# Kernel tuning notes

Hardware: AMD Instinct MI355X
Metric: run time of the kernel (lower is better)

Reference implementation:

```python
import jax, jax.numpy as jnp
import numpy as np

D = 128  # inputs / head dim

def setup_inputs() -> dict:
    key = jax.random.key(0)
    ks = jax.random.split(key, 7)
    B, S = 4, 4096
    s = 1.0 / np.sqrt(D)
    return {
        "x": jax.random.normal(ks[0], (B, S, D), dtype=jnp.float32),
        "Wq": jax.random.normal(ks[1], (D, D), dtype=jnp.float32) * s,
        "bq": jax.random.normal(ks[2], (D,), dtype=jnp.float32) * s,
        "Wk": jax.random.normal(ks[3], (D, D), dtype=jnp.float32) * s,
        "bk": jax.random.normal(ks[4], (D,), dtype=jnp.float32) * s,
        "Wv": jax.random.normal(ks[5], (D, D), dtype=jnp.float32) * s,
        "bv": jax.random.normal(ks[6], (D,), dtype=jnp.float32) * s,
    }

def reference(x, Wq, bq, Wk, bk, Wv, bv):
    B, S, d = x.shape
    # nn.Linear: y = x @ W^T + b
    q = jnp.einsum('bsd,ed->bse', x, Wq) + bq
    k = jnp.einsum('bsd,ed->bse', x, Wk) + bk
    v = jnp.einsum('bsd,ed->bse', x, Wv) + bv
    scores = jnp.einsum('bse,bte->bst', q, k) / jnp.sqrt(jnp.asarray(d, x.dtype))
    attn = jax.nn.softmax(scores, axis=-1)
    out = jnp.einsum('bst,bte->bse', attn, v)
    return out.reshape(B, S * d)
```

## Files before the change

### kernel.cpp

```cpp
#include <hip/hip_runtime.h>
#include <hip/hip_bf16.h>

typedef __bf16 bf16x8 __attribute__((ext_vector_type(8)));
typedef __bf16 bf16x4 __attribute__((ext_vector_type(4)));
typedef float  f32x4  __attribute__((ext_vector_type(4)));
typedef float  f32x16 __attribute__((ext_vector_type(16)));
typedef _Float16 f16x4 __attribute__((ext_vector_type(4)));

#define NB 4
#define SEQ 4096
#define DIM 128

static __device__ __forceinline__ unsigned int bf16bits(__bf16 h) {
    return (unsigned int)__builtin_bit_cast(unsigned short, h);
}

#define GLOAD_LDS16(g, s) __builtin_amdgcn_global_load_lds(                    \
    (const __attribute__((address_space(1))) void*)(g),                        \
    (__attribute__((address_space(3))) void*)(s), 16, 0, 0)

__global__ __launch_bounds__(256) void wconv(
    const float* __restrict__ Wq, const float* __restrict__ Wk,
    const float* __restrict__ Wv,
    __bf16* __restrict__ Wh, __bf16* __restrict__ Wl)
{
    int idx = blockIdx.x * 256 + threadIdx.x;
    int which = idx >> 12;
    int off = (idx & 4095) * 4;
    const float* W = which == 0 ? Wq : (which == 1 ? Wk : Wv);
    float4 v = *(const float4*)(W + off);
    bf16x4 h, lo;
    h[0] = (__bf16)v.x; h[1] = (__bf16)v.y; h[2] = (__bf16)v.z; h[3] = (__bf16)v.w;
    lo[0] = (__bf16)(v.x - (float)h[0]);
    lo[1] = (__bf16)(v.y - (float)h[1]);
    lo[2] = (__bf16)(v.z - (float)h[2]);
    lo[3] = (__bf16)(v.w - (float)h[3]);
    *(bf16x4*)(Wh + which * 16384 + off) = h;
    *(bf16x4*)(Wl + which * 16384 + off) = lo;
}

union QkvSh {
    float  xs[64][132];
    __bf16 vbuf[64][200];
};

__global__ __launch_bounds__(256) void qkv_proj3(
    const float* __restrict__ x,
    const __bf16* __restrict__ Whg, const __bf16* __restrict__ Wlg,
    const float* __restrict__ bq, const float* __restrict__ bk,
    const float* __restrict__ bv,
    __bf16* __restrict__ Q, __bf16* __restrict__ K, __bf16* __restrict__ Vt)
{
    __shared__ QkvSh sh;
    const int t  = threadIdx.x;
    const int w  = t >> 6, l = t & 63, lg = l >> 4, ll = l & 15;
    const int rt = blockIdx.x;
    const int ct0 = blockIdx.y * 12;

    {
        const float4* xsrc = (const float4*)(x + rt * 64 * 128);
        #pragma unroll
        for (int ii = 0; ii < 8; ++ii) {
            int u = t + ii * 256;
            float4 v4 = xsrc[u];
            *(float4*)&sh.xs[u >> 5][(u & 31) * 4] = v4;
        }
    }
    __syncthreads();

    float bfr[3];
    #pragma unroll
    for (int i = 0; i < 3; ++i) {
        int gct = ct0 + w * 3 + i;
        const float* bias = gct < 8 ? bq : (gct < 16 ? bk : bv);
        bfr[i] = bias[(gct & 7) * 16 + ll];
    }

    f32x4 acc[3][4];
    #pragma unroll
    for (int i = 0; i < 3; ++i)
        #pragma unroll
        for (int rf = 0; rf < 4; ++rf) acc[i][rf] = (f32x4){0.f, 0.f, 0.f, 0.f};

    #pragma unroll 1
    for (int kb = 0; kb < 4; ++kb) {
        bf16x8 xh[4], xl[4];
        #pragma unroll
        for (int rf = 0; rf < 4; ++rf) {
            float4 xa = *(const float4*)&sh.xs[rf * 16 + ll][kb * 32 + lg * 8];
            float4 xb = *(const float4*)&sh.xs[rf * 16 + ll][kb * 32 + lg * 8 + 4];
            float xv[8] = {xa.x, xa.y, xa.z, xa.w, xb.x, xb.y, xb.z, xb.w};
            #pragma unroll
            for (int j = 0; j < 8; ++j) {
                __bf16 h = (__bf16)xv[j];
                xh[rf][j] = h;
                xl[rf][j] = (__bf16)(xv[j] - (float)h);
            }
        }
        #pragma unroll
        for (int i = 0; i < 3; ++i) {
            int gct = ct0 + w * 3 + i;
            const __bf16* wb = Whg + (gct >> 3) * 16384 + ((gct & 7) * 16 + ll) * 128 + kb * 32 + lg * 8;
            const __bf16* lb = Wlg + (gct >> 3) * 16384 + ((gct & 7) * 16 + ll) * 128 + kb * 32 + lg * 8;
            bf16x8 wh = *(const bf16x8*)wb;
            bf16x8 wl = *(const bf16x8*)lb;
            #pragma unroll
            for (int rf = 0; rf < 4; ++rf) {
                acc[i][rf] = __builtin_amdgcn_mfma_f32_16x16x32_bf16(xh[rf], wh, acc[i][rf], 0, 0, 0);
                acc[i][rf] = __builtin_amdgcn_mfma_f32_16x16x32_bf16(xh[rf], wl, acc[i][rf], 0, 0, 0);
                acc[i][rf] = __builtin_amdgcn_mfma_f32_16x16x32_bf16(xl[rf], wh, acc[i][rf], 0, 0, 0);
            }
        }
    }

    __syncthreads();
    const float qscale = 0.08838834764831845f;
    #pragma unroll
    for (int i = 0; i < 3; ++i) {
        int gct = ct0 + w * 3 + i;
        float scale = (gct < 8) ? qscale : 1.0f;
        int lct = w * 3 + i;
        #pragma unroll
        for (int rf = 0; rf < 4; ++rf)
            #pragma unroll
            for (int r = 0; r < 4; ++r)
                sh.vbuf[rf * 16 + lg * 4 + r][lct * 16 + ll] =
                    (__bf16)((acc[i][rf][r] + bfr[i]) * scale);
    }
    __syncthreads();

    #pragma unroll 1
    for (int lct = 0; lct < 12; ++lct) {
        int gct = ct0 + lct;
        if (gct < 16) {
            int row = t >> 2, c = (t & 3) * 4;
            __bf16* base = (gct < 8 ? Q : K);
            bf16x4 v4 = *(const bf16x4*)&sh.vbuf[row][lct * 16 + c];
            *(bf16x4*)(base + (rt * 64 + row) * 128 + (gct & 7) * 16 + c) = v4;
        } else {
            int e = (gct - 16) * 16 + (t >> 4);
            int s0 = (t & 15) * 4;
            int bb = rt >> 6, sb = (rt & 63) * 64 + s0;
            bf16x4 v4;
            #pragma unroll
            for (int j = 0; j < 4; ++j) v4[j] = sh.vbuf[s0 + j][lct * 16 + (t >> 4)];
            *(bf16x4*)(Vt + bb * (128 * 4096) + e * 4096 + sb) = v4;
        }
    }
}

__global__ __launch_bounds__(256, 2) void attn_fwd(
    const __bf16* __restrict__ Qg,
    const __bf16* __restrict__ Kg,
    const __bf16* __restrict__ Vt,
    _Float16* __restrict__ Op, float* __restrict__ m_p, float* __restrict__ l_p,
    int kv_len)
{
    __shared__ __align__(16) __bf16 Kl[2][64][128];
    __shared__ __align__(16) __bf16 Vl[2][128][64];

    const int t  = threadIdx.x;
    const int w  = t >> 6;
    const int l  = t & 63;
    const int q  = l & 31;
    const int hi = l >> 5;
    const int s8 = l & 7;

    const int nwg = gridDim.x * gridDim.y;
    const int lin = blockIdx.x + gridDim.x * blockIdx.y;
    const int chunk = nwg >> 3;
    const int v = (lin & 7) * chunk + (lin >> 3);
    const int qt = v & 31;
    const int b  = (v >> 5) & 3;
    const int s  = v >> 7;

    const int qrow0 = qt * 128 + w * 32;

    bf16x8 qf[8];
    {
        const __bf16* qb = Qg + ((long)b * 4096 + qrow0 + q) * 128 + hi * 8;
        #pragma unroll
        for (int ks = 0; ks < 8; ++ks) qf[ks] = *(const bf16x8*)(qb + ks * 16);
    }

    f32x16 o32[4];
    #pragma unroll
    for (int dblk = 0; dblk < 4; ++dblk)
        #pragma unroll
        for (int r = 0; r < 16; ++r) o32[dblk][r] = 0.f;
    float m = -1e30f, lsum = 0.f;

    const __bf16* kbase = Kg + ((long)b * 4096 + s * kv_len) * 128;
    const __bf16* vbase = Vt + (long)b * 128 * 4096 + s * kv_len;

    int ksrc_off[4], vsrc_off[4];
    #pragma unroll
    for (int ii = 0; ii < 4; ++ii) {
        int u = w * 256 + ii * 64 + l;
        int kr = u >> 4, kc = u & 15;
        ksrc_off[ii] = kr * 128 + ((kc ^ (kr & 7)) * 8);
        int vr = u >> 3, vc = u & 7;
        vsrc_off[ii] = vr * 4096 + ((vc ^ (vr & 7)) * 8);
    }

    #define STAGE(kv, bp)                                                      \
    do {                                                                       \
        _Pragma("unroll")                                                      \
        for (int ii = 0; ii < 4; ++ii)                                         \
            GLOAD_LDS16(kbase + (long)(kv) * 128 + ksrc_off[ii],               \
                        (char*)&Kl[bp][0][0] + (w * 256 + ii * 64) * 16);      \
        _Pragma("unroll")                                                      \
        for (int ii = 0; ii < 4; ++ii)                                         \
            GLOAD_LDS16(vbase + (kv) + vsrc_off[ii],                           \
                        (char*)&Vl[bp][0][0] + (w * 256 + ii * 64) * 16);      \
    } while (0)

    STAGE(0, 0);
    asm volatile("s_waitcnt vmcnt(0)" ::: "memory");
    __syncthreads();

    const int nit = kv_len >> 6;
    int p = 0;
    for (int it = 0; it < nit; ++it) {
        if (it + 1 < nit) STAGE((it + 1) * 64, p ^ 1);

        f32x16 f0, f1;
        #pragma unroll
        for (int r = 0; r < 16; ++r) { f0[r] = 0.f; f1[r] = 0.f; }
        #pragma unroll
        for (int ks = 0; ks < 8; ++ks) {
            bf16x8 k0 = *(const bf16x8*)&Kl[p][q]     [(((ks * 2 + hi) ^ s8)) * 8];
            bf16x8 k1 = *(const bf16x8*)&Kl[p][32 + q][(((ks * 2 + hi) ^ s8)) * 8];
            f0 = __builtin_amdgcn_mfma_f32_32x32x16_bf16(k0, qf[ks], f0, 0, 0, 0);
            f1 = __builtin_amdgcn_mfma_f32_32x32x16_bf16(k1, qf[ks], f1, 0, 0, 0);
        }

        float mx = f0[0];
        #pragma unroll
        for (int r = 1; r < 16; ++r) mx = fmaxf(mx, f0[r]);
        #pragma unroll
        for (int r = 0; r < 16; ++r) mx = fmaxf(mx, f1[r]);
        mx = fmaxf(mx, __shfl_xor(mx, 32, 64));
        float mnew = fmaxf(m, mx);
        float alpha = __expf(m - mnew);
        m = mnew;

        float rsum = 0.f;
        unsigned int d0[8], d1[8];
        #pragma unroll
        for (int G = 0; G < 8; ++G) {
            int base = (G & 3) * 4;
            float pv[4];
            #pragma unroll
            for (int c = 0; c < 4; ++c) {
                float fv = (G >> 2) ? f1[base + c] : f0[base + c];
                pv[c] = __expf(fv - mnew);
            }
            __bf16 pb[4];
            #pragma unroll
            for (int c = 0; c < 4; ++c) { pb[c] = (__bf16)pv[c]; rsum += (float)pb[c]; }
            d0[G] = bf16bits(pb[0]) | (bf16bits(pb[1]) << 16);
            d1[G] = bf16bits(pb[2]) | (bf16bits(pb[3]) << 16);
        }
        lsum = lsum * alpha + rsum;

        #pragma unroll
        for (int dblk = 0; dblk < 4; ++dblk)
            #pragma unroll
            for (int r = 0; r < 16; ++r) o32[dblk][r] *= alpha;

        bf16x8 pf[4];
        #pragma unroll
        for (int k = 0; k < 4; ++k) {
            unsigned int a0 = d0[2 * k], b0 = d0[2 * k + 1];
            unsigned int a1 = d1[2 * k], b1 = d1[2 * k + 1];
            asm volatile("v_permlane32_swap_b32 %0, %1" : "+v"(a0), "+v"(b0));
            asm volatile("v_permlane32_swap_b32 %0, %1" : "+v"(a1), "+v"(b1));
            unsigned int dw[4] = {a0, a1, b0, b1};
            pf[k] = __builtin_bit_cast(bf16x8, *(uint4*)dw);
        }

        #pragma unroll
        for (int k = 0; k < 4; ++k) {
            #pragma unroll
            for (int dblk = 0; dblk < 4; ++dblk) {
                bf16x8 vf = *(const bf16x8*)&Vl[p][dblk * 32 + q][(((k * 2 + hi) ^ s8)) * 8];
                o32[dblk] = __builtin_amdgcn_mfma_f32_32x32x16_bf16(vf, pf[k], o32[dblk], 0, 0, 0);
            }
        }

        asm volatile("s_waitcnt vmcnt(0)" ::: "memory");
        __syncthreads();
        p ^= 1;
    }
    #undef STAGE

    long rowg = (long)s * (NB * SEQ) + b * 4096 + qrow0 + q;
    _Float16* op = Op + rowg * 128;
    #pragma unroll
    for (int dblk = 0; dblk < 4; ++dblk)
        #pragma unroll
        for (int d2 = 0; d2 < 4; ++d2)
            #pragma unroll
            for (int c = 0; c < 4; ++c)
                op[dblk * 32 + d2 * 8 + hi * 4 + c] = (_Float16)o32[dblk][d2 * 4 + c];
    lsum += __shfl_xor(lsum, 32, 64);
    if (hi == 0) {
        m_p[rowg] = m;
        l_p[rowg] = lsum;
    }
}

__global__ __launch_bounds__(256) void attn_merge(
    const _Float16* __restrict__ Op, const float* __restrict__ m_p,
    const float* __restrict__ l_p, float* __restrict__ out, int nsplit)
{
    const int t = threadIdx.x;
    const int base_row = blockIdx.x * 64;
    #pragma unroll 1
    for (int k = 0; k < 8; ++k) {
        int u = t + k * 256;
        int row = base_row + (u >> 5);
        int dq = u & 31;
        float M = -1e30f;
        for (int sp = 0; sp < nsplit; ++sp)
            M = fmaxf(M, m_p[(long)sp * (NB * SEQ) + row]);
        float L = 0.f;
        float4 acc = {0.f, 0.f, 0.f, 0.f};
        for (int sp = 0; sp < nsplit; ++sp) {
            long rb2 = (long)sp * (NB * SEQ) + row;
            float a = __expf(m_p[rb2] - M);
            L += l_p[rb2] * a;
            f16x4 vv = *(const f16x4*)(Op + rb2 * 128 + dq * 4);
            acc.x += (float)vv[0] * a; acc.y += (float)vv[1] * a;
            acc.z += (float)vv[2] * a; acc.w += (float)vv[3] * a;
        }
        float inv = 1.f / L;
        float4 r4 = {acc.x * inv, acc.y * inv, acc.z * inv, acc.w * inv};
        *(float4*)(out + (long)row * 128 + dq * 4) = r4;
    }
}

extern "C" void kernel_launch(void* const* d_in, const int* in_sizes, int n_in,
                              void* d_out, int out_size, void* d_ws, size_t ws_size,
                              hipStream_t stream) {
    (void)in_sizes; (void)n_in; (void)out_size;
    const float* x  = (const float*)d_in[0];
    const float* Wq = (const float*)d_in[1];
    const float* bq = (const float*)d_in[2];
    const float* Wk = (const float*)d_in[3];
    const float* bk = (const float*)d_in[4];
    const float* Wv = (const float*)d_in[5];
    const float* bv = (const float*)d_in[6];
    float* out = (float*)d_out;

    const size_t qkv_elems = (size_t)NB * SEQ * DIM;
    char* p = (char*)d_ws;
    __bf16* Q  = (__bf16*)p;        p += qkv_elems * 2;
    __bf16* K  = (__bf16*)p;        p += qkv_elems * 2;
    __bf16* Vt = (__bf16*)p;        p += qkv_elems * 2;
    __bf16* Wh = (__bf16*)p;        p += 3 * DIM * DIM * 2;
    __bf16* Wl = (__bf16*)p;        p += 3 * DIM * DIM * 2;
    size_t used = (size_t)(p - (char*)d_ws);

    const size_t per_split = (size_t)NB * SEQ * DIM * 2 + 2 * (size_t)NB * SEQ * 4;
    int nsplit = 4;
    while (nsplit > 1 && used + (size_t)nsplit * per_split > ws_size) nsplit >>= 1;

    _Float16* Op = (_Float16*)p;                 p += (size_t)nsplit * NB * SEQ * DIM * 2;
    float* m_p = (float*)p;                      p += (size_t)nsplit * NB * SEQ * 4;
    float* l_p = (float*)p;

    wconv<<<48, 256, 0, stream>>>(Wq, Wk, Wv, Wh, Wl);
    dim3 g1(256, 2);
    qkv_proj3<<<g1, 256, 0, stream>>>(x, Wh, Wl, bq, bk, bv, Q, K, Vt);
    dim3 g2(128, nsplit);
    attn_fwd<<<g2, 256, 0, stream>>>(Q, K, Vt, Op, m_p, l_p, SEQ / nsplit);
    attn_merge<<<256, 256, 0, stream>>>(Op, m_p, l_p, out, nsplit);
}
```

Baseline: 89.32 us.

## Halve attention KV tile to 32, raise occupancy and split-KV count

Shrinks the per-iteration K/V tile from 64 to 32 keys, which halves LDS usage and accumulator registers. It raises the launch-bounds occupancy hint to 4 blocks per CU and doubles the split-KV factor to 8 so more workgroups run in parallel. The V swizzle is reworked for the narrower 32-column rows. The cost is more loop iterations, each with its own barrier and online-softmax rescale, and more partial outputs for the merge kernel to read.

```diff
diff --git a/kernel.cpp b/kernel.cpp
--- a/kernel.cpp
+++ b/kernel.cpp
@@ -149,22 +149,23 @@
     }
 }
 
-__global__ __launch_bounds__(256, 2) void attn_fwd(
+__global__ __launch_bounds__(256, 4) void attn_fwd(
     const __bf16* __restrict__ Qg,
     const __bf16* __restrict__ Kg,
     const __bf16* __restrict__ Vt,
     _Float16* __restrict__ Op, float* __restrict__ m_p, float* __restrict__ l_p,
     int kv_len)
 {
-    __shared__ __align__(16) __bf16 Kl[2][64][128];
-    __shared__ __align__(16) __bf16 Vl[2][128][64];
+    __shared__ __align__(16) __bf16 Kl[2][32][128];
+    __shared__ __align__(16) __bf16 Vl[2][128][32];
 
     const int t  = threadIdx.x;
     const int w  = t >> 6;
     const int l  = t & 63;
     const int q  = l & 31;
     const int hi = l >> 5;
-    const int s8 = l & 7;
+    const int s8 = q & 7;
+    const int s4 = (q >> 1) & 3;
 
     const int nwg = gridDim.x * gridDim.y;
     const int lin = blockIdx.x + gridDim.x * blockIdx.y;
@@ -193,72 +194,65 @@
     const __bf16* kbase = Kg + ((long)b * 4096 + s * kv_len) * 128;
     const __bf16* vbase = Vt + (long)b * 128 * 4096 + s * kv_len;
 
-    int ksrc_off[4], vsrc_off[4];
-    #pragma unroll
-    for (int ii = 0; ii < 4; ++ii) {
-        int u = w * 256 + ii * 64 + l;
+    int ksrc_off[2], vsrc_off[2];
+    #pragma unroll
+    for (int ii = 0; ii < 2; ++ii) {
+        int u = (w * 2 + ii) * 64 + l;
         int kr = u >> 4, kc = u & 15;
         ksrc_off[ii] = kr * 128 + ((kc ^ (kr & 7)) * 8);
-        int vr = u >> 3, vc = u & 7;
-        vsrc_off[ii] = vr * 4096 + ((vc ^ (vr & 7)) * 8);
+        int vr = u >> 2, vc = u & 3;
+        vsrc_off[ii] = vr * 4096 + ((vc ^ ((vr >> 1) & 3)) * 8);
     }
 
     #define STAGE(kv, bp)                                                      \
     do {                                                                       \
         _Pragma("unroll")                                                      \
-        for (int ii = 0; ii < 4; ++ii)                                         \
+        for (int ii = 0; ii < 2; ++ii)                                         \
             GLOAD_LDS16(kbase + (long)(kv) * 128 + ksrc_off[ii],               \
-                        (char*)&Kl[bp][0][0] + (w * 256 + ii * 64) * 16);      \
+                        (char*)&Kl[bp][0][0] + (w * 2 + ii) * 1024);           \
         _Pragma("unroll")                                                      \
-        for (int ii = 0; ii < 4; ++ii)                                         \
+        for (int ii = 0; ii < 2; ++ii)                                         \
             GLOAD_LDS16(vbase + (kv) + vsrc_off[ii],                           \
-                        (char*)&Vl[bp][0][0] + (w * 256 + ii * 64) * 16);      \
+                        (char*)&Vl[bp][0][0] + (w * 2 + ii) * 1024);           \
     } while (0)
 
     STAGE(0, 0);
     asm volatile("s_waitcnt vmcnt(0)" ::: "memory");
     __syncthreads();
 
-    const int nit = kv_len >> 6;
+    const int nit = kv_len >> 5;
     int p = 0;
     for (int it = 0; it < nit; ++it) {
-        if (it + 1 < nit) STAGE((it + 1) * 64, p ^ 1);
-
-        f32x16 f0, f1;
-        #pragma unroll
-        for (int r = 0; r < 16; ++r) { f0[r] = 0.f; f1[r] = 0.f; }
+        if (it + 1 < nit) STAGE((it + 1) * 32, p ^ 1);
+
+        f32x16 f0;
+        #pragma unroll
+        for (int r = 0; r < 16; ++r) f0[r] = 0.f;
         #pragma unroll
         for (int ks = 0; ks < 8; ++ks) {
-            bf16x8 k0 = *(const bf16x8*)&Kl[p][q]     [(((ks * 2 + hi) ^ s8)) * 8];
-            bf16x8 k1 = *(const bf16x8*)&Kl[p][32 + q][(((ks * 2 + hi) ^ s8)) * 8];
+            bf16x8 k0 = *(const bf16x8*)&Kl[p][q][(((ks * 2 + hi) ^ s8)) * 8];
             f0 = __builtin_amdgcn_mfma_f32_32x32x16_bf16(k0, qf[ks], f0, 0, 0, 0);
-            f1 = __builtin_amdgcn_mfma_f32_32x32x16_bf16(k1, qf[ks], f1, 0, 0, 0);
         }
 
         float mx = f0[0];
         #pragma unroll
         for (int r = 1; r < 16; ++r) mx = fmaxf(mx, f0[r]);
-        #pragma unroll
-        for (int r = 0; r < 16; ++r) mx = fmaxf(mx, f1[r]);
         mx = fmaxf(mx, __shfl_xor(mx, 32, 64));
         float mnew = fmaxf(m, mx);
         float alpha = __expf(m - mnew);
         m = mnew;
 
         float rsum = 0.f;
-        unsigned int d0[8], d1[8];
-        #pragma unroll
-        for (int G = 0; G < 8; ++G) {
-            int base = (G & 3) * 4;
-            float pv[4];
+        unsigned int d0[4], d1[4];
+        #pragma unroll
+        for (int G = 0; G < 4; ++G) {
+            __bf16 pb[4];
             #pragma unroll
             for (int c = 0; c < 4; ++c) {
-                float fv = (G >> 2) ? f1[base + c] : f0[base + c];
-                pv[c] = __expf(fv - mnew);
+                float e = __expf(f0[G * 4 + c] - mnew);
+                pb[c] = (__bf16)e;
+                rsum += (float)pb[c];
             }
-            __bf16 pb[4];
-            #pragma unroll
-            for (int c = 0; c < 4; ++c) { pb[c] = (__bf16)pv[c]; rsum += (float)pb[c]; }
             d0[G] = bf16bits(pb[0]) | (bf16bits(pb[1]) << 16);
             d1[G] = bf16bits(pb[2]) | (bf16bits(pb[3]) << 16);
         }
@@ -269,9 +263,9 @@
             #pragma unroll
             for (int r = 0; r < 16; ++r) o32[dblk][r] *= alpha;
 
-        bf16x8 pf[4];
-        #pragma unroll
-        for (int k = 0; k < 4; ++k) {
+        bf16x8 pf[2];
+        #pragma unroll
+        for (int k = 0; k < 2; ++k) {
             unsigned int a0 = d0[2 * k], b0 = d0[2 * k + 1];
             unsigned int a1 = d1[2 * k], b1 = d1[2 * k + 1];
             asm volatile("v_permlane32_swap_b32 %0, %1" : "+v"(a0), "+v"(b0));
@@ -281,10 +275,10 @@
         }
 
         #pragma unroll
-        for (int k = 0; k < 4; ++k) {
+        for (int k = 0; k < 2; ++k) {
             #pragma unroll
             for (int dblk = 0; dblk < 4; ++dblk) {
-                bf16x8 vf = *(const bf16x8*)&Vl[p][dblk * 32 + q][(((k * 2 + hi) ^ s8)) * 8];
+                bf16x8 vf = *(const bf16x8*)&Vl[p][dblk * 32 + q][(((k * 2 + hi) ^ s4)) * 8];
                 o32[dblk] = __builtin_amdgcn_mfma_f32_32x32x16_bf16(vf, pf[k], o32[dblk], 0, 0, 0);
             }
         }
@@ -364,7 +358,7 @@
     size_t used = (size_t)(p - (char*)d_ws);
 
     const size_t per_split = (size_t)NB * SEQ * DIM * 2 + 2 * (size_t)NB * SEQ * 4;
-    int nsplit = 4;
+    int nsplit = 8;
     while (nsplit > 1 && used + (size_t)nsplit * per_split > ws_size) nsplit >>= 1;
 
     _Float16* Op = (_Float16*)p;                 p += (size_t)nsplit * NB * SEQ * DIM * 2;
```

Result: slower. 119.5 us (+33.8%).
